# Kernel tuning notes

Measured on AMD Instinct MI355X. Metric: run time of the kernel, lower is better.

Reference implementation:

```python
import jax, jax.numpy as jnp
import numpy as np

NIBBLE_ZERO = 8  # int4 zero-point (symmetric around 8 for unsigned nibble storage)


def _dequant(w_packed, w_scales):
    # w_packed: [out, in//2] int32 holding uint8 bytes, two 4-bit values each.
    low = w_packed & 0xF            # first nibble -> even input positions
    high = (w_packed >> 4) & 0xF    # second nibble -> odd input positions
    out_f = w_packed.shape[0]
    # interleave nibbles along the input dim: [out, in//2, 2] -> [out, in]
    q = jnp.stack([low, high], axis=-1).reshape(out_f, -1)
    return (q.astype(w_scales.dtype) - NIBBLE_ZERO) * w_scales[:, None]  # [out, in]


def setup_inputs() -> dict:
    key = jax.random.key(0)
    k1, k2, k3, k4 = jax.random.split(key, 4)
    N, IN, OUT = 4096, 4096, 4096
    x = jax.random.normal(k1, (N, IN), dtype=jnp.float32)
    w_packed = jax.random.randint(k2, (OUT, IN // 2), 0, 256, dtype=jnp.int32)
    w_scales = jax.random.uniform(k3, (OUT,), dtype=jnp.float32, minval=0.01, maxval=0.05)
    bias = jax.random.normal(k4, (OUT,), dtype=jnp.float32)
    return {"x": x, "w_packed": w_packed, "w_scales": w_scales, "bias": bias}


def reference(x, w_packed, w_scales, bias):
    W = _dequant(w_packed, w_scales)          # [out, in]
    return jnp.einsum('ni,oi->no', x, W) + bias  # [N, out]
```

## Files before the change

kernel.cpp:

```cpp
#include <hip/hip_runtime.h>
#include <hip/hip_bf16.h>


typedef __attribute__((ext_vector_type(8))) __bf16 bf16x8;
typedef __attribute__((ext_vector_type(4))) float f32x4;

#define GLOBAL_AS __attribute__((address_space(1)))
#define LDS_AS __attribute__((address_space(3)))

#define BM 256
#define BN 256
#define BK 64

__device__ inline unsigned short f32_to_bf16(float f) {
    unsigned int u = __float_as_uint(f);
    unsigned int r = (u + 0x7FFFu + ((u >> 16) & 1u)) >> 16;
    return (unsigned short)r;
}

__global__ void prep(const float* __restrict__ x, unsigned short* __restrict__ xb,
                     const int* __restrict__ wp, unsigned short* __restrict__ wb,
                     int n8x, int n4w) {
    const int stride = gridDim.x * blockDim.x;
    const int total = n8x + n4w;
    for (int i = blockIdx.x * blockDim.x + threadIdx.x; i < total; i += stride) {
        if (i < n8x) {
            float4 a = ((const float4*)x)[2 * i];
            float4 b = ((const float4*)x)[2 * i + 1];
            union { unsigned short h[8]; uint4 u; } o;
            o.h[0] = f32_to_bf16(a.x); o.h[1] = f32_to_bf16(a.y);
            o.h[2] = f32_to_bf16(a.z); o.h[3] = f32_to_bf16(a.w);
            o.h[4] = f32_to_bf16(b.x); o.h[5] = f32_to_bf16(b.y);
            o.h[6] = f32_to_bf16(b.z); o.h[7] = f32_to_bf16(b.w);
            ((uint4*)xb)[i] = o.u;
        } else {
            int k = i - n8x;
            int4 v = ((const int4*)wp)[k];
            int vals[4] = {v.x, v.y, v.z, v.w};
            union { unsigned short h[8]; uint4 u; } o;
#pragma unroll
            for (int t = 0; t < 4; ++t) {
                o.h[2 * t]     = f32_to_bf16((float)((vals[t] & 0xF) - 8));
                o.h[2 * t + 1] = f32_to_bf16((float)(((vals[t] >> 4) & 0xF) - 8));
            }
            ((uint4*)wb)[k] = o.u;
        }
    }
}

template<int K, int N>
__global__ __launch_bounds__(512, 2) void gemm_bt(
    const unsigned short* __restrict__ A,
    const unsigned short* __restrict__ B,
    const float* __restrict__ scales,
    const float* __restrict__ bias,
    float* __restrict__ C,
    int GY)
{
    constexpr int NT = K / BK;
    __shared__ __align__(16) unsigned short lds[65536];

    const int tid  = threadIdx.x;
    const int wave = tid >> 6;
    const int lane = tid & 63;
    const int wm = wave >> 2;
    const int wn = wave & 3;

    const int bid = blockIdx.x;
    const int chunk = gridDim.x >> 3;
    const int sw = (bid & 7) * chunk + (bid >> 3);
    const int bx = sw / GY;
    const int by = sw - bx * GY;
    const int m0 = by * BM;
    const int n0 = bx * BN;

    const int am = lane & 15;
    const int aq = lane >> 4;
    const int cb = ((aq ^ (am & 7)) << 4);

    int aoff[8], boff[4];
#pragma unroll
    for (int i = 0; i < 8; ++i) {
        int r = (2 * i + wm) * 16 + am;
        aoff[i] = ((i < 4) ? 0 : 16384) + (r & 127) * 128 + cb;
    }
#pragma unroll
    for (int j = 0; j < 4; ++j) {
        int r = (4 * j + wn) * 16 + am;
        boff[j] = 32768 + ((j < 2) ? 0 : 16384) + (r & 127) * 128 + cb;
    }

    const int sch = tid & 7;
    const int r0 = tid >> 3;
    const int r1 = (512 + tid) >> 3;
    const size_t g0 = (size_t)r0 * K + (size_t)((sch ^ (r0 & 7)) * 8);
    const size_t g1 = (size_t)r1 * K + (size_t)((sch ^ (r1 & 7)) * 8);
    const int d0 = tid * 8;
    const int d1 = (512 + tid) * 8;

    const unsigned short* Abase = A + (size_t)m0 * K;
    const unsigned short* Bbase = B + (size_t)n0 * K;

    f32x4 acc[8][4];
#pragma unroll
    for (int i = 0; i < 8; ++i)
#pragma unroll
        for (int j = 0; j < 4; ++j)
            acc[i][j] = (f32x4){0.f, 0.f, 0.f, 0.f};

    const char* ldsB = (const char*)lds;
    bf16x8 af[4][2], bfr[2][2];

#define STAGE(gbase, half, kcol, uoff)                                            \
    do {                                                                          \
        const unsigned short* _g = (gbase) + (size_t)((half) * 128) * K + (kcol); \
        __builtin_amdgcn_global_load_lds((const GLOBAL_AS void*)(_g + g0),        \
            (LDS_AS void*)(lds + (uoff) + d0), 16, 0, 0);                         \
        __builtin_amdgcn_global_load_lds((const GLOBAL_AS void*)(_g + g1),        \
            (LDS_AS void*)(lds + (uoff) + d1), 16, 0, 0);                         \
    } while (0)

#define LDA(mh, OB)                                                               \
    _Pragma("unroll") for (int i2 = 0; i2 < 4; ++i2) {                            \
        af[i2][0] = *(const bf16x8*)(ldsB + (OB) + aoff[(mh) * 4 + i2]);          \
        af[i2][1] = *(const bf16x8*)(ldsB + (OB) + (aoff[(mh) * 4 + i2] ^ 64));   \
    }

#define LDB(nh, OB)                                                               \
    _Pragma("unroll") for (int j2 = 0; j2 < 2; ++j2) {                            \
        bfr[j2][0] = *(const bf16x8*)(ldsB + (OB) + boff[(nh) * 2 + j2]);         \
        bfr[j2][1] = *(const bf16x8*)(ldsB + (OB) + (boff[(nh) * 2 + j2] ^ 64));  \
    }

#define BAR()  __builtin_amdgcn_s_barrier()

#define MFMA_Q(mh, nh)                                                            \
    _Pragma("unroll") for (int i2 = 0; i2 < 4; ++i2)                              \
    _Pragma("unroll") for (int j2 = 0; j2 < 2; ++j2) {                            \
        acc[(mh) * 4 + i2][(nh) * 2 + j2] = __builtin_amdgcn_mfma_f32_16x16x32_bf16( \
            af[i2][0], bfr[j2][0], acc[(mh) * 4 + i2][(nh) * 2 + j2], 0, 0, 0);   \
        acc[(mh) * 4 + i2][(nh) * 2 + j2] = __builtin_amdgcn_mfma_f32_16x16x32_bf16( \
            af[i2][1], bfr[j2][1], acc[(mh) * 4 + i2][(nh) * 2 + j2], 0, 0, 0);   \
    }

#define GROUP(OB, OUS, OUSo, t)                                                   \
    {                                                                             \
        const int kn1 = (((t) + 1 < NT) ? (t) + 1 : NT - 1) * BK;                 \
        const int kn2 = (((t) + 2 < NT) ? (t) + 2 : NT - 1) * BK;                 \
                \
        LDB(0, OB); LDA(0, OB);                                                   \
        STAGE(Bbase, 0, kn1, (OUSo) + 16384);                                     \
        BAR();                                                                    \
        __builtin_amdgcn_s_setprio(1); MFMA_Q(0, 0); __builtin_amdgcn_s_setprio(0); \
        __builtin_amdgcn_s_barrier();                                             \
                                                             \
        LDB(1, OB);                                                               \
        STAGE(Abase, 1, kn1, (OUSo) + 8192);                                      \
        BAR();                                                                    \
        __builtin_amdgcn_s_setprio(1); MFMA_Q(0, 1); __builtin_amdgcn_s_setprio(0); \
        __builtin_amdgcn_s_barrier();                                             \
                                                             \
        LDA(1, OB);                                                               \
        STAGE(Abase, 0, kn2, (OUS) + 0);                                          \
        BAR();                                                                    \
        __builtin_amdgcn_s_setprio(1); MFMA_Q(1, 1); __builtin_amdgcn_s_setprio(0); \
        __builtin_amdgcn_s_barrier();                                             \
                                                             \
        LDB(0, OB);                                                               \
        STAGE(Bbase, 1, kn2, (OUS) + 24576);                                      \
        asm volatile("s_waitcnt vmcnt(4)" ::: "memory");                          \
        BAR();                                                                    \
        __builtin_amdgcn_s_setprio(1); MFMA_Q(1, 0); __builtin_amdgcn_s_setprio(0); \
        __builtin_amdgcn_s_barrier();                                             \
    }

    STAGE(Abase, 0, 0, 0);
    STAGE(Bbase, 1, 0, 24576);
    STAGE(Bbase, 0, 0, 16384);
    STAGE(Abase, 1, 0, 8192);
    STAGE(Abase, 0, BK, 32768);
    STAGE(Bbase, 1, BK, 32768 + 24576);
    asm volatile("s_waitcnt vmcnt(4)" ::: "memory");
    __builtin_amdgcn_s_barrier();

    for (int t = 0; t < NT; t += 2) {
        GROUP(0, 0, 32768, t);
        GROUP(65536, 32768, 0, t + 1);
    }

    const int cq = lane >> 4;
    const int cc = lane & 15;
#pragma unroll
    for (int j = 0; j < 4; ++j) {
        const int col = n0 + (4 * j + wn) * 16 + cc;
        const float s = scales[col];
        const float b = bias[col];
#pragma unroll
        for (int i = 0; i < 8; ++i) {
            const int rowb = m0 + (2 * i + wm) * 16 + cq * 4;
#pragma unroll
            for (int r = 0; r < 4; ++r) {
                C[(size_t)(rowb + r) * N + col] = acc[i][j][r] * s + b;
            }
        }
    }
#undef STAGE
#undef LDA
#undef LDB
#undef BAR
#undef MFMA_Q
#undef GROUP
}

__global__ void naive_kernel(const float* __restrict__ x, const int* __restrict__ wp,
                             const float* __restrict__ sc, const float* __restrict__ bs,
                             float* __restrict__ out, int NR, int OUTF, int INF) {
    int idx = blockIdx.x * 256 + threadIdx.x;
    if (idx >= NR * OUTF) return;
    int n = idx / OUTF, o = idx - n * OUTF;
    const float* xr = x + (size_t)n * INF;
    const int* wr = wp + (size_t)o * (INF / 2);
    float acc = 0.f;
    for (int c = 0; c < INF / 2; ++c) {
        int v = wr[c];
        acc += xr[2 * c] * (float)((v & 0xF) - 8) + xr[2 * c + 1] * (float)(((v >> 4) & 0xF) - 8);
    }
    out[idx] = acc * sc[o] + bs[o];
}

extern "C" void kernel_launch(void* const* d_in, const int* in_sizes, int n_in,
                              void* d_out, int out_size, void* d_ws, size_t ws_size,
                              hipStream_t stream) {
    const float* x      = (const float*)d_in[0];
    const int*   wp     = (const int*)d_in[1];
    const float* scales = (const float*)d_in[2];
    const float* bias   = (const float*)d_in[3];
    float* out = (float*)d_out;

    const int OUTF = in_sizes[2];
    const int INF  = (2 * in_sizes[1]) / OUTF;
    const int NR   = in_sizes[0] / INF;

    unsigned short* xb = (unsigned short*)d_ws;
    unsigned short* wb = xb + (size_t)NR * INF;
    const size_t need = ((size_t)NR * INF + (size_t)OUTF * INF) * sizeof(unsigned short);

    const int GX = OUTF / BN;
    const int GY = NR / BM;

    if (ws_size >= need && INF == 4096 && OUTF == 4096 && (NR % BM) == 0
        && ((GX * GY) % 8) == 0
        && (in_sizes[0] % 8) == 0 && (in_sizes[1] % 4) == 0) {
        prep<<<2048, 256, 0, stream>>>(x, xb, wp, wb, in_sizes[0] / 8, in_sizes[1] / 4);
        gemm_bt<4096, 4096><<<GX * GY, 512, 0, stream>>>(xb, wb, scales, bias, out, GY);
    } else {
        int total = NR * OUTF;
        naive_kernel<<<(total + 255) / 256, 256, 0, stream>>>(x, wp, scales, bias, out, NR, OUTF, INF);
    }
}
```

Before: 266.5 us.

## Pre-swizzle dequantized weights into MFMA fragment order and load B directly to registers

The prep kernel now writes the bf16 weight matrix in a layout matching the per-lane MFMA B-fragment order. This lets the GEMM load B straight from global memory into registers instead of staging it through LDS. LDS now holds only the A tile, double-buffered, which halves the shared-memory footprint, and the four-phase barrier schedule becomes a simpler two-phase loop with a full vmcnt(0) wait per tile. The risks are exposed global-load latency on B, since only one register buffer is prefetched, and coarser synchronization. The fast path is also restricted to NR == 4096.

```diff
diff --git a/kernel.cpp b/kernel.cpp
--- a/kernel.cpp
+++ b/kernel.cpp
@@ -34,16 +34,24 @@
             o.h[6] = f32_to_bf16(b.z); o.h[7] = f32_to_bf16(b.w);
             ((uint4*)xb)[i] = o.u;
         } else {
-            int k = i - n8x;
-            int4 v = ((const int4*)wp)[k];
+            const int li = i - n8x;
+            const int l  = li & 63;
+            const int W  = li >> 6;
+            const int jb = W >> 7;
+            const int gb = W & 127;
+            const int am = l & 15, g4 = l >> 4;
+            const int o_ = jb * 16 + am;
+            const int g  = gb * 4 + g4;
+            int4 v = ((const int4*)wp)[(size_t)o_ * 512 + g];
             int vals[4] = {v.x, v.y, v.z, v.w};
-            union { unsigned short h[8]; uint4 u; } o;
-#pragma unroll
-            for (int t = 0; t < 4; ++t) {
-                o.h[2 * t]     = f32_to_bf16((float)((vals[t] & 0xF) - 8));
-                o.h[2 * t + 1] = f32_to_bf16((float)(((vals[t] >> 4) & 0xF) - 8));
+            union { unsigned short h[8]; uint4 u; } u8;
+#pragma unroll
+            for (int t2 = 0; t2 < 4; ++t2) {
+                u8.h[2 * t2]     = f32_to_bf16((float)((vals[t2] & 0xF) - 8));
+                u8.h[2 * t2 + 1] = f32_to_bf16((float)(((vals[t2] >> 4) & 0xF) - 8));
             }
-            ((uint4*)wb)[k] = o.u;
+            const int t_ = g >> 3, kk_ = (g >> 2) & 1, aq_ = g & 3;
+            ((uint4*)wb)[(jb << 13) | (t_ << 7) | (kk_ << 6) | (aq_ << 4) | am] = u8.u;
         }
     }
 }
@@ -51,14 +59,14 @@
 template<int K, int N>
 __global__ __launch_bounds__(512, 2) void gemm_bt(
     const unsigned short* __restrict__ A,
-    const unsigned short* __restrict__ B,
+    const unsigned short* __restrict__ Bf,
     const float* __restrict__ scales,
     const float* __restrict__ bias,
     float* __restrict__ C,
     int GY)
 {
     constexpr int NT = K / BK;
-    __shared__ __align__(16) unsigned short lds[65536];
+    __shared__ __align__(16) unsigned short lds[32768];
 
     const int tid  = threadIdx.x;
     const int wave = tid >> 6;
@@ -78,17 +86,18 @@
     const int aq = lane >> 4;
     const int cb = ((aq ^ (am & 7)) << 4);
 
-    int aoff[8], boff[4];
+    int aoff[8];
 #pragma unroll
     for (int i = 0; i < 8; ++i) {
         int r = (2 * i + wm) * 16 + am;
         aoff[i] = ((i < 4) ? 0 : 16384) + (r & 127) * 128 + cb;
     }
-#pragma unroll
-    for (int j = 0; j < 4; ++j) {
-        int r = (4 * j + wn) * 16 + am;
-        boff[j] = 32768 + ((j < 2) ? 0 : 16384) + (r & 127) * 128 + cb;
-    }
+
+    int bpan[4];
+#pragma unroll
+    for (int j = 0; j < 4; ++j)
+        bpan[j] = ((n0 >> 4) + 4 * j + wn) << 16;
+    const int lane8 = lane * 8;
 
     const int sch = tid & 7;
     const int r0 = tid >> 3;
@@ -99,7 +108,6 @@
     const int d1 = (512 + tid) * 8;
 
     const unsigned short* Abase = A + (size_t)m0 * K;
-    const unsigned short* Bbase = B + (size_t)n0 * K;
 
     f32x4 acc[8][4];
 #pragma unroll
@@ -109,84 +117,59 @@
             acc[i][j] = (f32x4){0.f, 0.f, 0.f, 0.f};
 
     const char* ldsB = (const char*)lds;
-    bf16x8 af[4][2], bfr[2][2];
-
-#define STAGE(gbase, half, kcol, uoff)                                            \
+    bf16x8 af8[8];
+    bf16x8 bX[4], bY[4];
+
+#define STAGE(half, kcol, uoff)                                                   \
     do {                                                                          \
-        const unsigned short* _g = (gbase) + (size_t)((half) * 128) * K + (kcol); \
+        const unsigned short* _g = Abase + (size_t)((half) * 128) * K + (kcol);   \
         __builtin_amdgcn_global_load_lds((const GLOBAL_AS void*)(_g + g0),        \
             (LDS_AS void*)(lds + (uoff) + d0), 16, 0, 0);                         \
         __builtin_amdgcn_global_load_lds((const GLOBAL_AS void*)(_g + g1),        \
             (LDS_AS void*)(lds + (uoff) + d1), 16, 0, 0);                         \
     } while (0)
 
-#define LDA(mh, OB)                                                               \
-    _Pragma("unroll") for (int i2 = 0; i2 < 4; ++i2) {                            \
-        af[i2][0] = *(const bf16x8*)(ldsB + (OB) + aoff[(mh) * 4 + i2]);          \
-        af[i2][1] = *(const bf16x8*)(ldsB + (OB) + (aoff[(mh) * 4 + i2] ^ 64));   \
-    }
-
-#define LDB(nh, OB)                                                               \
-    _Pragma("unroll") for (int j2 = 0; j2 < 2; ++j2) {                            \
-        bfr[j2][0] = *(const bf16x8*)(ldsB + (OB) + boff[(nh) * 2 + j2]);         \
-        bfr[j2][1] = *(const bf16x8*)(ldsB + (OB) + (boff[(nh) * 2 + j2] ^ 64));  \
-    }
-
-#define BAR()  __builtin_amdgcn_s_barrier()
-
-#define MFMA_Q(mh, nh)                                                            \
-    _Pragma("unroll") for (int i2 = 0; i2 < 4; ++i2)                              \
-    _Pragma("unroll") for (int j2 = 0; j2 < 2; ++j2) {                            \
-        acc[(mh) * 4 + i2][(nh) * 2 + j2] = __builtin_amdgcn_mfma_f32_16x16x32_bf16( \
-            af[i2][0], bfr[j2][0], acc[(mh) * 4 + i2][(nh) * 2 + j2], 0, 0, 0);   \
-        acc[(mh) * 4 + i2][(nh) * 2 + j2] = __builtin_amdgcn_mfma_f32_16x16x32_bf16( \
-            af[i2][1], bfr[j2][1], acc[(mh) * 4 + i2][(nh) * 2 + j2], 0, 0, 0);   \
-    }
-
-#define GROUP(OB, OUS, OUSo, t)                                                   \
+#define LDA_KK(kkv, OBb)                                                          \
+    _Pragma("unroll") for (int i2 = 0; i2 < 8; ++i2) {                            \
+        af8[i2] = *(const bf16x8*)(ldsB + (OBb) + (aoff[i2] ^ ((kkv) * 64)));     \
+    }
+
+#define LDBG(dst, TT2, kkv)                                                       \
+    _Pragma("unroll") for (int j2 = 0; j2 < 4; ++j2) {                            \
+        dst[j2] = *(const bf16x8*)(Bf + (size_t)bpan[j2] + (TT2) * 1024           \
+                                   + (kkv) * 512 + lane8);                        \
+    }
+
+#define MFMA_PH(bset)                                                             \
+    _Pragma("unroll") for (int i2 = 0; i2 < 8; ++i2)                              \
+    _Pragma("unroll") for (int j2 = 0; j2 < 4; ++j2)                              \
+        acc[i2][j2] = __builtin_amdgcn_mfma_f32_16x16x32_bf16(                    \
+            af8[i2], bset[j2], acc[i2][j2], 0, 0, 0);
+
+#define TILE(TT, OBb, OUSo)                                                       \
     {                                                                             \
-        const int kn1 = (((t) + 1 < NT) ? (t) + 1 : NT - 1) * BK;                 \
-        const int kn2 = (((t) + 2 < NT) ? (t) + 2 : NT - 1) * BK;                 \
-                \
-        LDB(0, OB); LDA(0, OB);                                                   \
-        STAGE(Bbase, 0, kn1, (OUSo) + 16384);                                     \
-        BAR();                                                                    \
-        __builtin_amdgcn_s_setprio(1); MFMA_Q(0, 0); __builtin_amdgcn_s_setprio(0); \
+        const int tn = (((TT) + 1 < NT) ? (TT) + 1 : NT - 1);                     \
+        asm volatile("s_waitcnt vmcnt(0)" ::: "memory");                          \
         __builtin_amdgcn_s_barrier();                                             \
-                                                             \
-        LDB(1, OB);                                                               \
-        STAGE(Abase, 1, kn1, (OUSo) + 8192);                                      \
-        BAR();                                                                    \
-        __builtin_amdgcn_s_setprio(1); MFMA_Q(0, 1); __builtin_amdgcn_s_setprio(0); \
-        __builtin_amdgcn_s_barrier();                                             \
-                                                             \
-        LDA(1, OB);                                                               \
-        STAGE(Abase, 0, kn2, (OUS) + 0);                                          \
-        BAR();                                                                    \
-        __builtin_amdgcn_s_setprio(1); MFMA_Q(1, 1); __builtin_amdgcn_s_setprio(0); \
-        __builtin_amdgcn_s_barrier();                                             \
-                                                             \
-        LDB(0, OB);                                                               \
-        STAGE(Bbase, 1, kn2, (OUS) + 24576);                                      \
-        asm volatile("s_waitcnt vmcnt(4)" ::: "memory");                          \
-        BAR();                                                                    \
-        __builtin_amdgcn_s_setprio(1); MFMA_Q(1, 0); __builtin_amdgcn_s_setprio(0); \
-        __builtin_amdgcn_s_barrier();                                             \
-    }
-
-    STAGE(Abase, 0, 0, 0);
-    STAGE(Bbase, 1, 0, 24576);
-    STAGE(Bbase, 0, 0, 16384);
-    STAGE(Abase, 1, 0, 8192);
-    STAGE(Abase, 0, BK, 32768);
-    STAGE(Bbase, 1, BK, 32768 + 24576);
-    asm volatile("s_waitcnt vmcnt(4)" ::: "memory");
-    __builtin_amdgcn_s_barrier();
+        LDBG(bY, (TT), 1);                             \
+        STAGE(0, tn * BK, (OUSo));                       \
+        STAGE(1, tn * BK, (OUSo) + 8192);                                         \
+        LDA_KK(0, OBb);                                                           \
+        __builtin_amdgcn_s_setprio(1); MFMA_PH(bX); __builtin_amdgcn_s_setprio(0);\
+        LDBG(bX, tn, 0);                            \
+        LDA_KK(1, OBb);                                                           \
+        __builtin_amdgcn_s_setprio(1); MFMA_PH(bY); __builtin_amdgcn_s_setprio(0);\
+    }
+
+    STAGE(0, 0, 0);
+    STAGE(1, 0, 8192);
+    LDBG(bX, 0, 0);
 
     for (int t = 0; t < NT; t += 2) {
-        GROUP(0, 0, 32768, t);
-        GROUP(65536, 32768, 0, t + 1);
-    }
+        TILE(t, 0, 16384);
+        TILE(t + 1, 32768, 0);
+    }
+    asm volatile("s_waitcnt vmcnt(0)" ::: "memory");
 
     const int cq = lane >> 4;
     const int cc = lane & 15;
@@ -205,11 +188,10 @@
         }
     }
 #undef STAGE
-#undef LDA
-#undef LDB
-#undef BAR
-#undef MFMA_Q
-#undef GROUP
+#undef LDA_KK
+#undef LDBG
+#undef MFMA_PH
+#undef TILE
 }
 
 __global__ void naive_kernel(const float* __restrict__ x, const int* __restrict__ wp,
@@ -248,7 +230,7 @@
     const int GX = OUTF / BN;
     const int GY = NR / BM;
 
-    if (ws_size >= need && INF == 4096 && OUTF == 4096 && (NR % BM) == 0
+    if (ws_size >= need && INF == 4096 && OUTF == 4096 && NR == 4096
         && ((GX * GY) % 8) == 0
         && (in_sizes[0] % 8) == 0 && (in_sizes[1] % 4) == 0) {
         prep<<<2048, 256, 0, stream>>>(x, xb, wp, wb, in_sizes[0] / 8, in_sizes[1] / 4);
```

New measurement: 272.8 us. 1.02x slower.
